# Kernel optimization log

Measured on AMD Instinct MI355X. Metric: run time of the kernel, lower is better.

The kernel has to match this reference:

```python
import jax, jax.numpy as jnp
import numpy as np

B = 128        # graphs per batch
N = 512        # nodes per graph (all graphs full-size)
F = 128        # input/hidden feature dim
DEG_AVG = 16   # average degree
E = B * N * DEG_AVG
DEGREES = (3, 3)  # polynomial filter order per conv layer


def setup_inputs() -> dict:
    key = jax.random.key(0)
    ks = jax.random.split(key, 8)
    X = jax.random.normal(ks[0], (B * N, F), dtype=jnp.float32)
    batch = jnp.repeat(jnp.arange(B, dtype=jnp.int32), N)
    # edges constrained within each graph: graph id = e // (N*DEG_AVG)
    gid = jnp.repeat(jnp.arange(B, dtype=jnp.int32), N * DEG_AVG)
    src = jax.random.randint(ks[1], (E,), 0, N, dtype=jnp.int32) + gid * N
    dst = jax.random.randint(ks[2], (E,), 0, N, dtype=jnp.int32) + gid * N
    edge_index = jnp.stack([src, dst], axis=0)
    s = 1.0 / np.sqrt(F)
    W1 = jax.random.normal(ks[3], (F, F), dtype=jnp.float32) * s
    b1 = jnp.zeros((F,), dtype=jnp.float32)
    W2 = jax.random.normal(ks[4], (F, F), dtype=jnp.float32) * s
    b2 = jnp.zeros((F,), dtype=jnp.float32)
    Wr1 = jax.random.normal(ks[5], (F, 64), dtype=jnp.float32) * s
    br1 = jnp.zeros((64,), dtype=jnp.float32)
    Wr2 = jax.random.normal(ks[6], (64, 1), dtype=jnp.float32) * (1.0 / 8.0)
    br2 = jnp.zeros((1,), dtype=jnp.float32)
    return {"X": X, "batch": batch, "edge_index": edge_index,
            "W1": W1, "b1": b1, "W2": W2, "b2": b2,
            "Wr1": Wr1, "br1": br1, "Wr2": Wr2, "br2": br2}


def _build_gso(edge_index):
    # dense per-graph adjacency [B, N, N] (block-diagonal global GSO,
    # represented batched for efficiency)
    g = edge_index[0] // N
    si = edge_index[0] % N
    di = edge_index[1] % N
    A = jnp.zeros((B, N, N), dtype=jnp.float32).at[g, si, di].set(1.0)
    # gso_generator: symmetric degree-normalized adjacency D^-1/2 A D^-1/2
    deg = A.sum(axis=-1)
    dinv = jnp.where(deg > 0, jax.lax.rsqrt(jnp.maximum(deg, 1e-12)), 0.0)
    S = dinv[:, :, None] * A * dinv[:, None, :]
    return S


def _poly_conv(S, x, degree, W, b):
    # sum_{k=0..degree} S^k x, then linear projection
    acc = x
    z = x
    for _ in range(degree):
        z = jnp.einsum('bij,bjf->bif', S, z)
        acc = acc + z
    return jnp.einsum('bnf,fo->bno', acc, W) + b


def reference(X, batch, edge_index, W1, b1, W2, b2, Wr1, br1, Wr2, br2):
    S = _build_gso(edge_index)
    x = X.reshape(B, N, F)  # nodes grouped per graph (batch is sorted)
    x = jax.nn.relu(_poly_conv(S, x, DEGREES[0], W1, b1))
    x = jax.nn.relu(_poly_conv(S, x, DEGREES[1], W2, b2))
    # global mean pool over nodes of each graph
    h = x.mean(axis=1)  # [B, F]
    h = jax.nn.relu(h @ Wr1 + br1)
    out = (h @ Wr2 + br2).squeeze(-1)  # [B]
    return out
```

## Files before the change

kernel.cpp:

```cpp
#include <hip/hip_runtime.h>
#include <hip/hip_bf16.h>

#define NB 128
#define NN 512
#define NF 128
#define BN (NB*NN)
#define NE (BN*16)
#define EPG 8192
#define WPR 16
#define ELLW 64
#define QST 32
#define SST 72
#define WTS 136

typedef short sh8 __attribute__((ext_vector_type(8)));
typedef float f32x4 __attribute__((ext_vector_type(4)));

static __device__ __forceinline__ unsigned short f2bf(float f) {
    unsigned u = __float_as_uint(f);
    u += 0x7fffu + ((u >> 16) & 1u);
    return (unsigned short)(u >> 16);
}

#define DOT2LO(acc_, pk_, one_) \
    asm("v_dot2_f32_bf16 %0, %1, %2, %0" : "+v"(acc_) : "v"(pk_), "v"(one_))

__global__ __launch_bounds__(1024) void build_fused_kernel(
    const int* __restrict__ src, const int* __restrict__ dst,
    unsigned short* __restrict__ ell, int* __restrict__ ocnt,
    float* __restrict__ dinvr, int* __restrict__ perm)
{
    __shared__ unsigned bm[NN * WPR];
    __shared__ unsigned short els[256 * SST];
    __shared__ int qp[NN * 4];
    __shared__ int cs[NN];
    __shared__ int rdeg[NN];
    __shared__ int irank[NN];
    __shared__ int prow[NN];
    int* prk = (int*)els;
    int b = blockIdx.x;
    int g = b >> 1;
    int h = b & 1;
    int t = threadIdx.x;

    for (int i = t; i < NN * WPR; i += 1024) bm[i] = 0u;
    __syncthreads();

    const int4* sg4 = (const int4*)(src + (size_t)g * EPG);
    const int4* dg4 = (const int4*)(dst + (size_t)g * EPG);
    for (int i = t; i < EPG / 4; i += 1024) {
        int4 s4 = sg4[i];
        int4 d4 = dg4[i];
        int s, d;
        s = s4.x & (NN - 1); d = d4.x & (NN - 1);
        atomicOr(&bm[s * WPR + (d >> 5)], 1u << (d & 31));
        s = s4.y & (NN - 1); d = d4.y & (NN - 1);
        atomicOr(&bm[s * WPR + (d >> 5)], 1u << (d & 31));
        s = s4.z & (NN - 1); d = d4.z & (NN - 1);
        atomicOr(&bm[s * WPR + (d >> 5)], 1u << (d & 31));
        s = s4.w & (NN - 1); d = d4.w & (NN - 1);
        atomicOr(&bm[s * WPR + (d >> 5)], 1u << (d & 31));
    }
    __syncthreads();

    {
        int r = t & 511, hf = t >> 9;
        const unsigned* bgr = &bm[r * WPR + hf * 8];
        uint4 a = *(const uint4*)bgr;
        uint4 c = *(const uint4*)(bgr + 4);
        qp[r * 4 + hf * 2]     = __popc(a.x) + __popc(a.y) + __popc(a.z) + __popc(a.w);
        qp[r * 4 + hf * 2 + 1] = __popc(c.x) + __popc(c.y) + __popc(c.z) + __popc(c.w);
    }
    __syncthreads();
    if (t < NN) {
        int d = qp[t * 4] + qp[t * 4 + 1] + qp[t * 4 + 2] + qp[t * 4 + 3];
        cs[t] = (d > ELLW) ? ELLW : d;
    }
    __syncthreads();

    {
        int r = t & 511, hf = t >> 9;
        int deg_r = cs[r];
        const int4* c4 = (const int4*)cs;
        int ib = hf * 64;
        int pcnt = 0;
        #pragma unroll 8
        for (int ii = 0; ii < 64; ++ii) {
            int4 v = c4[ib + ii];
            int i0 = (ib + ii) * 4;
            pcnt += (v.x < deg_r) || (v.x == deg_r && (i0 + 0) < r);
            pcnt += (v.y < deg_r) || (v.y == deg_r && (i0 + 1) < r);
            pcnt += (v.z < deg_r) || (v.z == deg_r && (i0 + 2) < r);
            pcnt += (v.w < deg_r) || (v.w == deg_r && (i0 + 3) < r);
        }
        if (!hf) prk[r] = pcnt;
        __syncthreads();
        if (hf) {
            int rk = prk[r] + pcnt;
            irank[r] = rk;
            rdeg[rk] = deg_r;
            prow[rk] = r;
            if (h == 0) {
                perm[(size_t)g * NN + rk] = r;
                dinvr[(size_t)g * NN + rk] =
                    (deg_r > 0) ? rsqrtf((float)deg_r) : 0.0f;
            }
        }
    }
    __syncthreads();

    if (h == 0 && t < NN / 8) {
        int m = rdeg[t * 8 + 7];
        ocnt[(size_t)g * (NN / 8) + t] = (m + 3) & ~3;
    }

    {
        int rkl = t >> 2;
        int qw  = t & 3;
        int rk  = h * 256 + rkl;
        int row = prow[rk];
        uint4 bv = *(const uint4*)&bm[row * WPR + qw * 4];
        unsigned wbits[4] = {bv.x, bv.y, bv.z, bv.w};
        int c = 0;
        #pragma unroll
        for (int j = 0; j < 3; ++j) c += (j < qw) ? qp[row * 4 + j] : 0;
        unsigned short* er = &els[rkl * SST];
        #pragma unroll
        for (int w = 0; w < 4; ++w) {
            unsigned bits = wbits[w];
            while (bits) {
                int j = __ffs(bits) - 1;
                bits &= bits - 1;
                if (c < ELLW) er[c] = (unsigned short)irank[(qw * 4 + w) * 32 + j];
                ++c;
            }
        }
        if (qw == 3) {
            int cc = (c > ELLW) ? ELLW : c;
            for (int p = cc; p < ELLW; ++p) er[p] = (unsigned short)NN;
        }
    }
    __syncthreads();

    unsigned short* outb = ell + ((size_t)g * NN + (size_t)h * 256) * ELLW;
    for (int idx = t; idx < 256 * 8; idx += 1024) {
        int r2 = idx >> 3, sg2 = idx & 7;
        uint4 v = *(const uint4*)&els[r2 * SST + sg2 * 8];
        *(uint4*)&outb[(size_t)r2 * ELLW + sg2 * 8] = v;
    }
}

__global__ __launch_bounds__(512, 4) void poly_fused_kernel(
    const float* __restrict__ xin,
    unsigned short* __restrict__ accout,
    const unsigned short* __restrict__ ell,
    const int* __restrict__ ocnt,
    const float* __restrict__ dinvr,
    const int* __restrict__ perm,
    int permuteIn)
{
    extern __shared__ float lds[];
    unsigned short* w = (unsigned short*)lds;
    float* dsh = lds + ((NN + 1) * QST * 2) / 4;

    int b = blockIdx.x;
    int g = b & 127;
    int q = b >> 7;
    int t = threadIdx.x;
    int wid = t >> 6;
    int qd  = (t >> 2) & 15;
    int fbq = t & 3;

    unsigned one_lo = 0x00003F80u;
    unsigned one_hi = 0x3F800000u;

    if (t < NN) dsh[t] = dinvr[(size_t)g * NN + t];
    if (t < QST) w[NN * QST + t] = 0;

    int rnk[4];
    #pragma unroll
    for (int x = 0; x < 4; ++x) {
        int wl = (x >= 2) ? (7 - wid) : wid;
        rnk[x] = x * 128 + wl * 16 + qd;
    }

    const int* oc = ocnt + (size_t)g * (NN / 8);
    int co[4];
    #pragma unroll
    for (int x = 0; x < 4; ++x) {
        int ob = (rnk[x] - qd) >> 3;
        co[x] = __builtin_amdgcn_readfirstlane(max(oc[ob], oc[ob + 1]));
    }

    int px[4];
    if (permuteIn) {
        const int* pmg = perm + (size_t)g * NN;
        #pragma unroll
        for (int x = 0; x < 4; ++x) px[x] = pmg[rnk[x]];
    } else {
        #pragma unroll
        for (int x = 0; x < 4; ++x) px[x] = rnk[x];
    }

    const float* xg = xin + (size_t)g * NN * NF + q * 32 + fbq * 8;

    float acc[4][8];
    #pragma unroll
    for (int x = 0; x < 4; ++x) {
        int row = px[x];
        float4 a0 = *(const float4*)&xg[(size_t)row * NF];
        float4 a1 = *(const float4*)&xg[(size_t)row * NF + 4];
        acc[x][0] = a0.x; acc[x][1] = a0.y; acc[x][2] = a0.z; acc[x][3] = a0.w;
        acc[x][4] = a1.x; acc[x][5] = a1.y; acc[x][6] = a1.z; acc[x][7] = a1.w;
    }

    __syncthreads();

    #pragma unroll
    for (int x = 0; x < 4; ++x) {
        float di = dsh[rnk[x]];
        unsigned pk[4];
        #pragma unroll
        for (int k = 0; k < 4; ++k) {
            unsigned lo = (unsigned)f2bf(di * acc[x][2 * k]);
            unsigned hi = (unsigned)f2bf(di * acc[x][2 * k + 1]);
            pk[k] = lo | (hi << 16);
        }
        *(uint4*)&w[rnk[x] * QST + fbq * 8] = make_uint4(pk[0], pk[1], pk[2], pk[3]);
    }
    __syncthreads();

    for (int hop = 0; hop < 3; ++hop) {
        unsigned pst[4][4];
        #pragma unroll
        for (int x = 0; x < 4; ++x) {
            const unsigned short* el =
                ell + ((size_t)g * NN + rnk[x]) * ELLW;
            int cnt = co[x];
            float s[8];
            #pragma unroll
            for (int k = 0; k < 8; ++k) s[k] = 0.0f;

            ushort4 cur = *(const ushort4*)el;
            for (int p = 0; p < cnt; p += 4) {
                ushort4 nxt = cur;
                if (p + 4 < cnt) nxt = *(const ushort4*)(el + p + 4);
                uint4 v0 = *(const uint4*)&w[(int)cur.x * QST + fbq * 8];
                uint4 v1 = *(const uint4*)&w[(int)cur.y * QST + fbq * 8];
                uint4 v2 = *(const uint4*)&w[(int)cur.z * QST + fbq * 8];
                uint4 v3 = *(const uint4*)&w[(int)cur.w * QST + fbq * 8];
                unsigned d[4][4] = {{v0.x, v0.y, v0.z, v0.w},
                                    {v1.x, v1.y, v1.z, v1.w},
                                    {v2.x, v2.y, v2.z, v2.w},
                                    {v3.x, v3.y, v3.z, v3.w}};
                #pragma unroll
                for (int n = 0; n < 4; ++n) {
                    #pragma unroll
                    for (int k = 0; k < 4; ++k) {
                        DOT2LO(s[2 * k],     d[n][k], one_lo);
                        DOT2LO(s[2 * k + 1], d[n][k], one_hi);
                    }
                }
                cur = nxt;
            }

            float di = dsh[rnk[x]];
            #pragma unroll
            for (int k = 0; k < 4; ++k) {
                float zlo = di * s[2 * k];
                float zhi = di * s[2 * k + 1];
                acc[x][2 * k]     += zlo;
                acc[x][2 * k + 1] += zhi;
                unsigned lo = (unsigned)f2bf(di * zlo);
                unsigned hi = (unsigned)f2bf(di * zhi);
                pst[x][k] = lo | (hi << 16);
            }
        }
        __syncthreads();
        #pragma unroll
        for (int x = 0; x < 4; ++x) {
            *(uint4*)&w[rnk[x] * QST + fbq * 8] =
                make_uint4(pst[x][0], pst[x][1], pst[x][2], pst[x][3]);
        }
        __syncthreads();
    }

    unsigned short* og = accout + (size_t)g * NN * NF + q * 32 + fbq * 8;
    #pragma unroll
    for (int x = 0; x < 4; ++x) {
        int rr = rnk[x];
        uint4 pk;
        pk.x = (unsigned)f2bf(acc[x][0]) | ((unsigned)f2bf(acc[x][1]) << 16);
        pk.y = (unsigned)f2bf(acc[x][2]) | ((unsigned)f2bf(acc[x][3]) << 16);
        pk.z = (unsigned)f2bf(acc[x][4]) | ((unsigned)f2bf(acc[x][5]) << 16);
        pk.w = (unsigned)f2bf(acc[x][6]) | ((unsigned)f2bf(acc[x][7]) << 16);
        *(uint4*)&og[(size_t)rr * NF] = pk;
    }
}

__global__ __launch_bounds__(256, 2) void gemm_bias_relu_kernel(
    const unsigned short* __restrict__ X,
    const float* __restrict__ W,
    const float* __restrict__ b, float* __restrict__ Y,
    float* __restrict__ partial, int fuse)
{
    __shared__ __align__(16) unsigned short Wt[NF * WTS];
    __shared__ float part[4 * NF];

    int t = threadIdx.x;

    for (int i = t; i < NF * NF / 4; i += 256) {
        int k = i >> 5;
        int n4 = (i & 31) * 4;
        float4 wv = ((const float4*)W)[i];
        Wt[(n4 + 0) * WTS + k] = f2bf(wv.x);
        Wt[(n4 + 1) * WTS + k] = f2bf(wv.y);
        Wt[(n4 + 2) * WTS + k] = f2bf(wv.z);
        Wt[(n4 + 3) * WTS + k] = f2bf(wv.w);
    }
    __syncthreads();

    int lane = t & 63;
    int wid  = t >> 6;
    int quad = lane >> 4;
    int l16  = lane & 15;
    int rowA0 = blockIdx.x * 128 + wid * 32;

    union { uint4 q; sh8 v; } af[2][4];
    #pragma unroll
    for (int m = 0; m < 2; ++m) {
        int r = rowA0 + m * 16 + l16;
        const unsigned short* xr = X + (size_t)r * NF + quad * 8;
        #pragma unroll
        for (int kk = 0; kk < 4; ++kk)
            af[m][kk].q = *(const uint4*)(xr + kk * 32);
    }

    f32x4 acc[2][8];
    #pragma unroll
    for (int m = 0; m < 2; ++m)
        #pragma unroll
        for (int c = 0; c < 8; ++c) acc[m][c] = (f32x4){0.f, 0.f, 0.f, 0.f};

    #pragma unroll
    for (int c = 0; c < 8; ++c) {
        const unsigned short* wb = &Wt[(c * 16 + l16) * WTS + quad * 8];
        #pragma unroll
        for (int kk = 0; kk < 4; ++kk) {
            union { uint4 q; sh8 v; } bf_;
            bf_.q = *(const uint4*)(wb + kk * 32);
            acc[0][c] = __builtin_amdgcn_mfma_f32_16x16x32_bf16(
                af[0][kk].v, bf_.v, acc[0][c], 0, 0, 0);
            acc[1][c] = __builtin_amdgcn_mfma_f32_16x16x32_bf16(
                af[1][kk].v, bf_.v, acc[1][c], 0, 0, 0);
        }
    }

    float psum[8];
    #pragma unroll
    for (int c = 0; c < 8; ++c) psum[c] = 0.0f;

    #pragma unroll
    for (int c = 0; c < 8; ++c) {
        int col = c * 16 + l16;
        float bias = b[col];
        #pragma unroll
        for (int m = 0; m < 2; ++m) {
            #pragma unroll
            for (int reg = 0; reg < 4; ++reg) {
                int r = rowA0 + m * 16 + quad * 4 + reg;
                float v = fmaxf(acc[m][c][reg] + bias, 0.0f);
                if (!fuse) Y[(size_t)r * NF + col] = v;
                psum[c] += v;
            }
        }
    }

    if (fuse) {
        #pragma unroll
        for (int c = 0; c < 8; ++c) {
            float v = psum[c];
            v += __shfl_xor(v, 16);
            v += __shfl_xor(v, 32);
            if (lane < 16) part[wid * NF + c * 16 + lane] = v;
        }
        __syncthreads();
        if (t < NF) {
            float s = part[t] + part[NF + t] + part[2 * NF + t]
                    + part[3 * NF + t];
            partial[(size_t)blockIdx.x * NF + t] = s;
        }
    }
}

__global__ __launch_bounds__(128) void readout_kernel(
    const float* __restrict__ partial,
    const float* __restrict__ Wr1, const float* __restrict__ br1,
    const float* __restrict__ Wr2, const float* __restrict__ br2,
    float* __restrict__ out)
{
    __shared__ float hsh[NF];
    __shared__ float r1[64];

    int g = blockIdx.x;
    int t = threadIdx.x;

    const float* pg = partial + (size_t)g * 4 * NF;
    float s = 0.0f;
    #pragma unroll
    for (int j = 0; j < 4; ++j) s += pg[j * NF + t];
    hsh[t] = s * (1.0f / (float)NN);
    __syncthreads();

    if (t < 64) {
        float a = br1[t];
        #pragma unroll 8
        for (int k = 0; k < NF; ++k) a += hsh[k] * Wr1[k * 64 + t];
        r1[t] = fmaxf(a, 0.0f);
    }
    __syncthreads();

    if (t < 64) {
        float v = r1[t] * Wr2[t];
        #pragma unroll
        for (int off = 32; off; off >>= 1) v += __shfl_down(v, off);
        if (t == 0) out[g] = v + br2[0];
    }
}

extern "C" void kernel_launch(void* const* d_in, const int* in_sizes, int n_in,
                              void* d_out, int out_size, void* d_ws, size_t ws_size,
                              hipStream_t stream)
{
    const float* X    = (const float*)d_in[0];
    const int*   ei   = (const int*)d_in[2];
    const float* W1   = (const float*)d_in[3];
    const float* b1   = (const float*)d_in[4];
    const float* W2   = (const float*)d_in[5];
    const float* b2   = (const float*)d_in[6];
    const float* Wr1  = (const float*)d_in[7];
    const float* br1  = (const float*)d_in[8];
    const float* Wr2  = (const float*)d_in[9];
    const float* br2  = (const float*)d_in[10];
    float* out = (float*)d_out;

    const int* src = ei;
    const int* dst = ei + NE;

    char* ws = (char*)d_ws;
    float*          dinvr   = (float*)(ws);
    int*            ocnt    = (int*)(ws + (size_t)256 * 1024);
    int*            perm    = (int*)(ws + (size_t)512 * 1024);
    float*          partial = (float*)(ws + (size_t)768 * 1024);
    unsigned short* ell     = (unsigned short*)(ws + (size_t)1024 * 1024);
    unsigned short* buf0    = (unsigned short*)(ws + (size_t)16384 * 1024);
    float*          buf1    = (float*)(ws + (size_t)49152 * 1024);

    build_fused_kernel<<<NB * 2, 1024, 0, stream>>>(src, dst, ell, ocnt,
                                                    dinvr, perm);

    const size_t LDSSZ = (size_t)(NN + 1) * QST * 2 + NN * 4;

    poly_fused_kernel<<<NB * 4, 512, LDSSZ, stream>>>(X, buf0, ell, ocnt,
                                                      dinvr, perm, 1);
    gemm_bias_relu_kernel<<<BN / 128, 256, 0, stream>>>(buf0, W1, b1, buf1,
                                                        partial, 0);

    poly_fused_kernel<<<NB * 4, 512, LDSSZ, stream>>>(buf1, buf0, ell, ocnt,
                                                      dinvr, perm, 0);
    gemm_bias_relu_kernel<<<BN / 128, 256, 0, stream>>>(buf0, W2, b2, buf1,
                                                        partial, 1);

    readout_kernel<<<NB, 128, 0, stream>>>(partial, Wr1, br1, Wr2, br2, out);
}
```

Before: 212.5 us.

## Widen poly kernel feature slice to 64 with 1024-thread blocks

```diff
diff --git a/kernel.cpp b/kernel.cpp
--- a/kernel.cpp
+++ b/kernel.cpp
@@ -9,7 +9,7 @@
 #define EPG 8192
 #define WPR 16
 #define ELLW 64
-#define QST 32
+#define QST 64
 #define SST 72
 #define WTS 136
 
@@ -150,7 +150,7 @@
     }
 }
 
-__global__ __launch_bounds__(512, 4) void poly_fused_kernel(
+__global__ __launch_bounds__(1024, 2) void poly_fused_kernel(
     const float* __restrict__ xin,
     unsigned short* __restrict__ accout,
     const unsigned short* __restrict__ ell,
@@ -167,9 +167,9 @@
     int g = b & 127;
     int q = b >> 7;
     int t = threadIdx.x;
+    int fb8 = t & 7;
+    int rs  = t >> 3;
     int wid = t >> 6;
-    int qd  = (t >> 2) & 15;
-    int fbq = t & 3;
 
     unsigned one_lo = 0x00003F80u;
     unsigned one_hi = 0x3F800000u;
@@ -179,18 +179,13 @@
 
     int rnk[4];
     #pragma unroll
-    for (int x = 0; x < 4; ++x) {
-        int wl = (x >= 2) ? (7 - wid) : wid;
-        rnk[x] = x * 128 + wl * 16 + qd;
-    }
+    for (int x = 0; x < 4; ++x) rnk[x] = x * 128 + rs;
 
     const int* oc = ocnt + (size_t)g * (NN / 8);
     int co[4];
     #pragma unroll
-    for (int x = 0; x < 4; ++x) {
-        int ob = (rnk[x] - qd) >> 3;
-        co[x] = __builtin_amdgcn_readfirstlane(max(oc[ob], oc[ob + 1]));
-    }
+    for (int x = 0; x < 4; ++x)
+        co[x] = __builtin_amdgcn_readfirstlane(oc[x * 16 + wid]);
 
     int px[4];
     if (permuteIn) {
@@ -202,7 +197,7 @@
         for (int x = 0; x < 4; ++x) px[x] = rnk[x];
     }
 
-    const float* xg = xin + (size_t)g * NN * NF + q * 32 + fbq * 8;
+    const float* xg = xin + (size_t)g * NN * NF + q * 64 + fb8 * 8;
 
     float acc[4][8];
     #pragma unroll
@@ -226,7 +221,7 @@
             unsigned hi = (unsigned)f2bf(di * acc[x][2 * k + 1]);
             pk[k] = lo | (hi << 16);
         }
-        *(uint4*)&w[rnk[x] * QST + fbq * 8] = make_uint4(pk[0], pk[1], pk[2], pk[3]);
+        *(uint4*)&w[rnk[x] * QST + fb8 * 8] = make_uint4(pk[0], pk[1], pk[2], pk[3]);
     }
     __syncthreads();
 
@@ -245,10 +240,10 @@
             for (int p = 0; p < cnt; p += 4) {
                 ushort4 nxt = cur;
                 if (p + 4 < cnt) nxt = *(const ushort4*)(el + p + 4);
-                uint4 v0 = *(const uint4*)&w[(int)cur.x * QST + fbq * 8];
-                uint4 v1 = *(const uint4*)&w[(int)cur.y * QST + fbq * 8];
-                uint4 v2 = *(const uint4*)&w[(int)cur.z * QST + fbq * 8];
-                uint4 v3 = *(const uint4*)&w[(int)cur.w * QST + fbq * 8];
+                uint4 v0 = *(const uint4*)&w[(int)cur.x * QST + fb8 * 8];
+                uint4 v1 = *(const uint4*)&w[(int)cur.y * QST + fb8 * 8];
+                uint4 v2 = *(const uint4*)&w[(int)cur.z * QST + fb8 * 8];
+                uint4 v3 = *(const uint4*)&w[(int)cur.w * QST + fb8 * 8];
                 unsigned d[4][4] = {{v0.x, v0.y, v0.z, v0.w},
                                     {v1.x, v1.y, v1.z, v1.w},
                                     {v2.x, v2.y, v2.z, v2.w},
@@ -279,13 +274,13 @@
         __syncthreads();
         #pragma unroll
         for (int x = 0; x < 4; ++x) {
-            *(uint4*)&w[rnk[x] * QST + fbq * 8] =
+            *(uint4*)&w[rnk[x] * QST + fb8 * 8] =
                 make_uint4(pst[x][0], pst[x][1], pst[x][2], pst[x][3]);
         }
         __syncthreads();
     }
 
-    unsigned short* og = accout + (size_t)g * NN * NF + q * 32 + fbq * 8;
+    unsigned short* og = accout + (size_t)g * NN * NF + q * 64 + fb8 * 8;
     #pragma unroll
     for (int x = 0; x < 4; ++x) {
         int rr = rnk[x];
@@ -461,13 +456,13 @@
 
     const size_t LDSSZ = (size_t)(NN + 1) * QST * 2 + NN * 4;
 
-    poly_fused_kernel<<<NB * 4, 512, LDSSZ, stream>>>(X, buf0, ell, ocnt,
-                                                      dinvr, perm, 1);
+    poly_fused_kernel<<<NB * 2, 1024, LDSSZ, stream>>>(X, buf0, ell, ocnt,
+                                                       dinvr, perm, 1);
     gemm_bias_relu_kernel<<<BN / 128, 256, 0, stream>>>(buf0, W1, b1, buf1,
                                                         partial, 0);
 
-    poly_fused_kernel<<<NB * 4, 512, LDSSZ, stream>>>(buf1, buf0, ell, ocnt,
-                                                      dinvr, perm, 0);
+    poly_fused_kernel<<<NB * 2, 1024, LDSSZ, stream>>>(buf1, buf0, ell, ocnt,
+                                                       dinvr, perm, 0);
     gemm_bias_relu_kernel<<<BN / 128, 256, 0, stream>>>(buf0, W2, b2, buf1,
                                                         partial, 1);
 
```

New measurement: 214.4 us. About the same (+0.9%).
